# Optimization experiments

Hardware: AMD Instinct MI355X
Metric: run time of the kernel (lower is better)

The kernel has to match this reference:

```python
import jax, jax.numpy as jnp
import numpy as np

EPS_BN = 1e-5
EPS_LN = 1e-5

def _bn(x, g, b, m, v):
    # inference-mode BatchNorm2d over channel dim 1
    scale = g / jnp.sqrt(v + EPS_BN)
    return x * scale[None, :, None, None] + (b - m * scale)[None, :, None, None]

def _conv1x1(x, w, b=None):
    y = jnp.einsum('bchw,oc->bohw', x, w)
    if b is not None:
        y = y + b[None, :, None, None]
    return y

def _gelu(x):
    return jax.nn.gelu(x, approximate=False)

def setup_inputs() -> dict:
    key = jax.random.key(0)
    ks = jax.random.split(key, 40)
    B, C, H, W = 32, 160, 56, 56
    C5, C3 = C // 5, C * 3
    s = 0.05
    d = {}
    d['x'] = jax.random.normal(ks[0], (B, C, H, W), jnp.float32)
    d['bn1_g'] = jax.random.uniform(ks[1], (C,), jnp.float32, 0.5, 1.5)
    d['bn1_b'] = jax.random.normal(ks[2], (C,)) * s
    d['bn1_m'] = jax.random.normal(ks[3], (C,)) * s
    d['bn1_v'] = jnp.ones((C,), jnp.float32)
    names = ['t', 'b', 'r', 'l', 'c']
    for i, n in enumerate(names):
        d['w' + n] = jax.random.normal(ks[4 + i], (C5, C)) * s
        d['b' + n] = jax.random.normal(ks[9 + i], (C5,)) * s
    d['wf1'] = jax.random.normal(ks[14], (C, C)) * s
    d['bf1'] = jax.random.normal(ks[15], (C,)) * s
    d['bn2_g'] = jax.random.uniform(ks[16], (C,), jnp.float32, 0.5, 1.5)
    d['bn2_b'] = jax.random.normal(ks[17], (C,)) * s
    d['bn2_m'] = jax.random.normal(ks[18], (C,)) * s
    d['bn2_v'] = jnp.ones((C,), jnp.float32)
    d['wph'] = jax.random.normal(ks[19], (W, W)) * s
    d['bph'] = jax.random.normal(ks[20], (W,)) * s
    d['wpw'] = jax.random.normal(ks[21], (H, H)) * s
    d['bpw'] = jax.random.normal(ks[22], (H,)) * s
    d['wf2'] = jax.random.normal(ks[23], (C, C3)) * s
    d['ln_g'] = jax.random.uniform(ks[24], (C,), jnp.float32, 0.5, 1.5)
    d['ln_b'] = jax.random.normal(ks[25], (C,)) * s
    d['wfc1'] = jax.random.normal(ks[26], (C3, C)) * s
    d['bfc1'] = jax.random.normal(ks[27], (C3,)) * s
    d['wfc2'] = jax.random.normal(ks[28], (C, C3)) * s
    d['bfc2'] = jax.random.normal(ks[29], (C,)) * s
    d['step'] = 1
    return d

def reference(x, bn1_g, bn1_b, bn1_m, bn1_v, wt, bt, wb, bb, wr, br, wl, bl, wc, bc,
              wf1, bf1, bn2_g, bn2_b, bn2_m, bn2_v, wph, bph, wpw, bpw, wf2,
              ln_g, ln_b, wfc1, bfc1, wfc2, bfc2, step):
    B, C, H, W = x.shape
    # ---- localMix: ShiftedPillarsConcatentation_BNAct_NP5 ----
    h = _gelu(_bn(x, bn1_g, bn1_b, bn1_m, bn1_v))
    x_t = _conv1x1(h, wt, bt)
    x_b = _conv1x1(h, wb, bb)
    x_r = _conv1x1(h, wr, br)
    x_l = _conv1x1(h, wl, bl)
    x_c = _conv1x1(h, wc, bc)
    # pad then narrow exactly as torch: t/l shift by 1, b/r shift by step
    x_t = jnp.pad(x_t, ((0, 0), (0, 0), (0, step), (0, 0)))[:, :, 1:1 + H, :]
    x_b = jnp.pad(x_b, ((0, 0), (0, 0), (step, 0), (0, 0)))[:, :, 0:H, :]
    x_l = jnp.pad(x_l, ((0, 0), (0, 0), (0, 0), (0, step)))[:, :, :, 1:1 + W]
    x_r = jnp.pad(x_r, ((0, 0), (0, 0), (0, 0), (step, 0)))[:, :, :, 0:W]
    lm = _conv1x1(jnp.concatenate([x_t, x_b, x_r, x_l, x_c], axis=1), wf1, bf1)
    # ---- globalMix: sparseMLP_BNAct ----
    g = _gelu(_bn(lm, bn2_g, bn2_b, bn2_m, bn2_v))
    # proj_h mixes the W axis (input permuted to (B,W,C,H)), bias per output W
    x_h = jnp.einsum('bchw,vw->bchv', g, wph) + bph[None, None, None, :]
    # proj_w mixes the H axis (input permuted to (B,H,C,W)), bias per output H
    x_w = jnp.einsum('bchw,uh->bcuw', g, wpw) + bpw[None, None, :, None]
    gm = _conv1x1(jnp.concatenate([g, x_h, x_w], axis=1), wf2)  # no bias
    x1 = gm + x  # residual 1
    # ---- channelMix: LN + Mlp over channels ----
    y = jnp.transpose(x1, (0, 2, 3, 1))  # BHWC
    mu = jnp.mean(y, axis=-1, keepdims=True)
    var = jnp.mean(jnp.square(y - mu), axis=-1, keepdims=True)
    y = (y - mu) / jnp.sqrt(var + EPS_LN) * ln_g + ln_b
    y = _gelu(jnp.einsum('bhwc,fc->bhwf', y, wfc1) + bfc1)
    y = jnp.einsum('bhwf,cf->bhwc', y, wfc2) + bfc2
    return jnp.transpose(y, (0, 3, 1, 2)) + x1  # residual 2
```

## Files before the change

kernel.cpp:

```cpp
#include <hip/hip_runtime.h>
#include <hip/hip_bf16.h>
#include <math.h>

typedef __hip_bfloat16 bf16;
typedef __attribute__((ext_vector_type(8))) short s8v;
typedef __attribute__((ext_vector_type(4))) float f4v;
typedef __attribute__((ext_vector_type(4))) unsigned short u4v;

#define Bn  32
#define Cn  160
#define HWn 3136
#define Pn  100352

__device__ __forceinline__ float b2f(bf16 v){ return __bfloat162float(v); }
__device__ __forceinline__ bf16  f2b(float v){ return __float2bfloat16(v); }
__device__ __forceinline__ float bits2f(unsigned short u){
    union { float f; unsigned int i; } x; x.i = ((unsigned int)u) << 16; return x.f;
}
__device__ __forceinline__ unsigned short f2bits(float v){
    union { unsigned short us; bf16 b; } cv; cv.b = f2b(v); return cv.us;
}
__device__ __forceinline__ float gelu_f(float x){
    float ax = fabsf(x) * 0.7071067811865476f;
    float t  = 1.0f / (1.0f + 0.3275911f*ax);
    float p  = ((((1.061405429f*t - 1.453152027f)*t + 1.421413741f)*t
                 - 0.284496736f)*t + 0.254829592f)*t;
    float e  = __expf(-ax*ax);
    float erfv = 1.0f - p*e;
    float s = (x >= 0.f) ? erfv : -erfv;
    return 0.5f*x*(1.0f + s);
}

#define MFMA(a,b,c) __builtin_amdgcn_mfma_f32_16x16x32_bf16((a),(b),(c),0,0,0)

__global__ __launch_bounds__(256) void k0_prep(
    const float* __restrict__ wt, const float* __restrict__ wb_, const float* __restrict__ wr,
    const float* __restrict__ wl, const float* __restrict__ wc,
    const float* __restrict__ bt, const float* __restrict__ bb_, const float* __restrict__ br,
    const float* __restrict__ bl, const float* __restrict__ bc,
    const float* __restrict__ wf1, const float* __restrict__ bf1,
    const float* __restrict__ g2, const float* __restrict__ b2, const float* __restrict__ m2, const float* __restrict__ v2,
    const float* __restrict__ wf2, const float* __restrict__ wfc1, const float* __restrict__ wfc2,
    const float* __restrict__ wph, const float* __restrict__ wpw,
    const float* __restrict__ lng, const float* __restrict__ lnb, const float* __restrict__ bfc1,
    bf16* wcat, bf16* wf1b, bf16* wf2b, bf16* wfc1g, bf16* wfc2b, bf16* wphb, bf16* wpwb,
    float* bcat, float* epsv, float* eptv, float* wgs, float* wcb)
{
    int idx = blockIdx.x*256 + threadIdx.x;
    if (idx < 25600){ int o = idx/160, k = idx - o*160; int gi = o>>5, oo = o&31;
        const float* wp = gi==0?wt: gi==1?wb_: gi==2?wr: gi==3?wl: wc;
        wcat[idx] = f2b(wp[oo*160+k]); return; }
    idx -= 25600;
    if (idx < 25600){ wf1b[idx] = f2b(wf1[idx]); return; }
    idx -= 25600;
    if (idx < 76800){ wf2b[idx] = f2b(wf2[idx]); return; }
    idx -= 76800;
    if (idx < 76800){ int f = idx/160, c = idx - f*160;
        wfc1g[idx] = f2b(wfc1[f*160+c] * lng[c]); return; }
    idx -= 76800;
    if (idx < 76800){ wfc2b[idx] = f2b(wfc2[idx]); return; }
    idx -= 76800;
    if (idx < 4096){ int v = idx>>6, w = idx&63;
        wphb[idx] = (v<56 && w<56) ? f2b(wph[v*56+w]) : f2b(0.f); return; }
    idx -= 4096;
    if (idx < 4096){ int v = idx>>6, w = idx&63;
        wpwb[idx] = (v<56 && w<56) ? f2b(wpw[v*56+w]) : f2b(0.f); return; }
    idx -= 4096;
    if (idx < 160){ int o = idx; int gi = o>>5, oo = o&31;
        const float* bp = gi==0?bt: gi==1?bb_: gi==2?br: gi==3?bl: bc;
        bcat[o] = bp[oo]; return; }
    idx -= 160;
    if (idx < 160){ int o = idx; float s = g2[o]*rsqrtf(v2[o]+1e-5f);
        epsv[o] = s; eptv[o] = (bf1[o]-m2[o])*s + b2[o]; return; }
    idx -= 160;
    if (idx < 480){ int o = idx; float sg = 0.f, sb = 0.f;
        const float* wr_ = wfc1 + (size_t)o*160;
        for (int c = 0; c < 160; ++c){ float w = wr_[c]; sg += w*lng[c]; sb += w*lnb[c]; }
        wgs[o] = sg; wcb[o] = sb + bfc1[o]; return; }
}

__global__ __launch_bounds__(256) void k1_bn_gelu_tr(const float* __restrict__ x,
    const float* __restrict__ g, const float* __restrict__ b,
    const float* __restrict__ m, const float* __restrict__ v,
    bf16* __restrict__ hT)
{
    __shared__ float tile[64*161];
    __shared__ float sc[160], sh[160];
    int blk = blockIdx.x; int bb = blk/49; int hw0 = (blk - bb*49)*64;
    int tid = threadIdx.x;
    if (tid < 160){
        float s = g[tid] * rsqrtf(v[tid] + 1e-5f);
        sc[tid] = s; sh[tid] = b[tid] - m[tid]*s;
    }
    __syncthreads();
    const float* xb = x + (size_t)bb*Cn*HWn + hw0;
    for (int idx = tid; idx < 160*64; idx += 256){
        int c = idx >> 6, p = idx & 63;
        float val = xb[(size_t)c*HWn + p];
        tile[p*161 + c] = gelu_f(val*sc[c] + sh[c]);
    }
    __syncthreads();
    bf16* ho = hT + ((size_t)bb*HWn + hw0)*Cn;
    for (int idx = tid; idx < 64*160; idx += 256){
        int p = idx/160, c = idx - p*160;
        ho[idx] = f2b(tile[p*161 + c]);
    }
}

__global__ __launch_bounds__(256) void k2_conv5(const bf16* __restrict__ hT,
    const bf16* __restrict__ wcat, const float* __restrict__ bcat, bf16* __restrict__ y5T)
{
    __shared__ __align__(16) unsigned short Bs[2][16*168];
    int tid = threadIdx.x, wave = tid>>6, lane = tid&63, m = lane&15, q = lane>>4;
    size_t pos0 = (size_t)blockIdx.x*64;
    const unsigned short* Ap = (const unsigned short*)hT + (pos0 + wave*16 + m)*160 + q*8;
    s8v a[5];
    #pragma unroll
    for (int kb = 0; kb < 5; ++kb) a[kb] = *(const s8v*)(Ap + kb*32);
    { const s8v* sp = (const s8v*)((const unsigned short*)wcat);
      for (int c = tid; c < 320; c += 256){ int row = c/20, col = (c - row*20)*8;
          *(s8v*)&Bs[0][row*168 + col] = sp[c]; } }
    __syncthreads();
    for (int s = 0; s < 10; ++s){
        if (s+1 < 10){
            const s8v* sp = (const s8v*)((const unsigned short*)wcat + (size_t)(s+1)*2560);
            for (int c = tid; c < 320; c += 256){ int row = c/20, col = (c - row*20)*8;
                *(s8v*)&Bs[(s+1)&1][row*168 + col] = sp[c]; }
        }
        f4v acc = {0.f,0.f,0.f,0.f};
        const unsigned short* Bp = &Bs[s&1][m*168 + q*8];
        #pragma unroll
        for (int kb = 0; kb < 5; ++kb) acc = MFMA(a[kb], *(const s8v*)(Bp + kb*32), acc);
        float bias = bcat[s*16 + m];
        bf16* yo = y5T + (pos0 + wave*16 + q*4)*160 + s*16 + m;
        #pragma unroll
        for (int r = 0; r < 4; ++r) yo[r*160] = f2b(acc[r] + bias);
        __syncthreads();
    }
}

__global__ __launch_bounds__(256) void k3_wf1(const bf16* __restrict__ y5T,
    const bf16* __restrict__ wf1b, const float* __restrict__ epsv, const float* __restrict__ eptv,
    bf16* __restrict__ gT)
{
    __shared__ __align__(16) unsigned short Bs[2][16*168];
    int tid = threadIdx.x, wave = tid>>6, lane = tid&63, m = lane&15, q = lane>>4;
    int blk = blockIdx.x; int bb = blk/49; int hw0 = (blk - bb*49)*64;
    size_t pos0 = (size_t)bb*HWn + hw0;
    int phw = hw0 + wave*16 + m; int h = phw/56, w = phw - h*56;
    s8v a[5];
    #pragma unroll
    for (int kb = 0; kb < 5; ++kb){
        int h2 = h, w2 = w; bool ok = true;
        if      (kb == 0){ h2 = h+1; ok = (h2 < 56); }
        else if (kb == 1){ h2 = h-1; ok = (h2 >= 0); }
        else if (kb == 2){ w2 = w-1; ok = (w2 >= 0); }
        else if (kb == 3){ w2 = w+1; ok = (w2 < 56); }
        if (ok){
            const unsigned short* Ap = (const unsigned short*)y5T +
                ((size_t)bb*HWn + h2*56 + w2)*160 + kb*32 + q*8;
            a[kb] = *(const s8v*)Ap;
        } else {
            a[kb] = (s8v){0,0,0,0,0,0,0,0};
        }
    }
    { const s8v* sp = (const s8v*)((const unsigned short*)wf1b);
      for (int c = tid; c < 320; c += 256){ int row = c/20, col = (c - row*20)*8;
          *(s8v*)&Bs[0][row*168 + col] = sp[c]; } }
    __syncthreads();
    for (int s = 0; s < 10; ++s){
        if (s+1 < 10){
            const s8v* sp = (const s8v*)((const unsigned short*)wf1b + (size_t)(s+1)*2560);
            for (int c = tid; c < 320; c += 256){ int row = c/20, col = (c - row*20)*8;
                *(s8v*)&Bs[(s+1)&1][row*168 + col] = sp[c]; }
        }
        f4v acc = {0.f,0.f,0.f,0.f};
        const unsigned short* Bp = &Bs[s&1][m*168 + q*8];
        #pragma unroll
        for (int kb = 0; kb < 5; ++kb) acc = MFMA(a[kb], *(const s8v*)(Bp + kb*32), acc);
        int o = s*16 + m;
        float es = epsv[o], et = eptv[o];
        bf16* go = gT + (pos0 + wave*16 + q*4)*160 + o;
        #pragma unroll
        for (int r = 0; r < 4; ++r) go[r*160] = f2b(gelu_f(acc[r]*es + et));
        __syncthreads();
    }
}

__global__ __launch_bounds__(256) void k4_projh(const bf16* __restrict__ gT,
    const bf16* __restrict__ wphb, const float* __restrict__ bph, bf16* __restrict__ xhT)
{
    __shared__ __align__(16) unsigned short gS[160*72];
    int tid = threadIdx.x, wave = tid>>6, lane = tid&63, m = lane&15, q = lane>>4;
    int blk = blockIdx.x; int b = blk/56, h = blk - b*56;
    const unsigned short* ga = (const unsigned short*)gT + ((size_t)b*HWn + h*56)*160;
    for (int idx = tid; idx < 56*160; idx += 256){
        int w = idx/160, c = idx - w*160;
        gS[c*72 + w] = ga[idx];
    }
    for (int idx = tid; idx < 160*8; idx += 256){
        int c = idx>>3, w = 56 + (idx&7);
        gS[c*72 + w] = 0;
    }
    __syncthreads();
    int v0 = wave*16;
    s8v a[2];
    #pragma unroll
    for (int kb = 0; kb < 2; ++kb)
        a[kb] = *(const s8v*)((const unsigned short*)wphb + (v0+m)*64 + kb*32 + q*8);
    int v = v0 + q*4;
    for (int s = 0; s < 10; ++s){
        f4v acc = {0.f,0.f,0.f,0.f};
        const unsigned short* Bp = &gS[(s*16+m)*72 + q*8];
        #pragma unroll
        for (int kb = 0; kb < 2; ++kb) acc = MFMA(a[kb], *(const s8v*)(Bp + kb*32), acc);
        #pragma unroll
        for (int r = 0; r < 4; ++r){
            int vv = v + r;
            if (vv < 56)
                xhT[((size_t)b*HWn + h*56 + vv)*160 + s*16 + m] = f2b(acc[r] + bph[vv]);
        }
    }
}

__global__ __launch_bounds__(256) void k5_projw(const bf16* __restrict__ gT,
    const bf16* __restrict__ wpwb, const float* __restrict__ bpw, bf16* __restrict__ xwT)
{
    __shared__ __align__(16) unsigned short gS[160*72];
    int tid = threadIdx.x, wave = tid>>6, lane = tid&63, m = lane&15, q = lane>>4;
    int blk = blockIdx.x; int b = blk/56, w = blk - b*56;
    const unsigned short* gbase = (const unsigned short*)gT + ((size_t)b*HWn + w)*160;
    for (int idx = tid; idx < 56*160; idx += 256){
        int hh = idx/160, c = idx - hh*160;
        gS[c*72 + hh] = gbase[(size_t)hh*56*160 + c];
    }
    for (int idx = tid; idx < 160*8; idx += 256){
        int c = idx>>3, hh = 56 + (idx&7);
        gS[c*72 + hh] = 0;
    }
    __syncthreads();
    int v0 = wave*16;
    s8v a[2];
    #pragma unroll
    for (int kb = 0; kb < 2; ++kb)
        a[kb] = *(const s8v*)((const unsigned short*)wpwb + (v0+m)*64 + kb*32 + q*8);
    int v = v0 + q*4;
    for (int s = 0; s < 10; ++s){
        f4v acc = {0.f,0.f,0.f,0.f};
        const unsigned short* Bp = &gS[(s*16+m)*72 + q*8];
        #pragma unroll
        for (int kb = 0; kb < 2; ++kb) acc = MFMA(a[kb], *(const s8v*)(Bp + kb*32), acc);
        #pragma unroll
        for (int r = 0; r < 4; ++r){
            int vv = v + r;
            if (vv < 56)
                xwT[((size_t)b*HWn + vv*56 + w)*160 + s*16 + m] = f2b(acc[r] + bpw[vv]);
        }
    }
}

__global__ __launch_bounds__(256) void k6_wf2(const bf16* __restrict__ gT,
    const bf16* __restrict__ xhT, const bf16* __restrict__ xwT,
    const bf16* __restrict__ wf2b, bf16* __restrict__ gm)
{
    __shared__ __align__(16) unsigned short Bs[2][16*488];
    int tid = threadIdx.x, wave = tid>>6, lane = tid&63, m = lane&15, q = lane>>4;
    size_t pos0 = (size_t)blockIdx.x*64;
    size_t prow = (pos0 + wave*16 + m)*160;
    s8v a[15];
    #pragma unroll
    for (int kb = 0; kb < 15; ++kb){
        const bf16* src = (kb < 5) ? gT : (kb < 10 ? xhT : xwT);
        int kc = (kb - (kb < 5 ? 0 : (kb < 10 ? 5 : 10)))*32 + q*8;
        a[kb] = *(const s8v*)((const unsigned short*)src + prow + kc);
    }
    { const s8v* sp = (const s8v*)((const unsigned short*)wf2b);
      for (int c = tid; c < 960; c += 256){ int row = c/60, col = (c - row*60)*8;
          *(s8v*)&Bs[0][row*488 + col] = sp[c]; } }
    __syncthreads();
    for (int s = 0; s < 10; ++s){
        if (s+1 < 10){
            const s8v* sp = (const s8v*)((const unsigned short*)wf2b + (size_t)(s+1)*7680);
            for (int c = tid; c < 960; c += 256){ int row = c/60, col = (c - row*60)*8;
                *(s8v*)&Bs[(s+1)&1][row*488 + col] = sp[c]; }
        }
        f4v acc = {0.f,0.f,0.f,0.f};
        const unsigned short* Bp = &Bs[s&1][m*488 + q*8];
        #pragma unroll
        for (int kb = 0; kb < 15; ++kb) acc = MFMA(a[kb], *(const s8v*)(Bp + kb*32), acc);
        bf16* go = gm + (pos0 + wave*16 + q*4)*160 + s*16 + m;
        #pragma unroll
        for (int r = 0; r < 4; ++r) go[r*160] = f2b(acc[r]);
        __syncthreads();
    }
}

__global__ __launch_bounds__(256,3) void k78_mlp(const float* __restrict__ x,
    const bf16* __restrict__ gm,
    const bf16* __restrict__ wfc1g, const float* __restrict__ wcb,
    const bf16* __restrict__ wfc2b, const float* __restrict__ bfc2,
    float* __restrict__ out)
{
    __shared__ __align__(16) char lds[40960];
    float* Xs = (float*)lds;
    char* UsB = lds;
    char* AsB = lds + 30720;

    int tid = threadIdx.x, wave = tid>>6, lane = tid&63, m = lane&15, q = lane>>4;
    int rt = wave&1, chh = wave>>1;
    int blk = blockIdx.x; int bb = blk/98; int hw0 = (blk - bb*98)*32;
    size_t pos0 = (size_t)bb*HWn + hw0;
    const float* xb = x + (size_t)bb*Cn*HWn + hw0;

    for (int idx = tid; idx < 160*32; idx += 256){
        int c = idx >> 5, p = idx & 31;
        Xs[p*164 + c] = xb[(size_t)c*HWn + p];
    }
    __syncthreads();

    {
        int p = tid >> 3, q8 = tid & 7; int c0 = q8*20;
        const unsigned short* gp = (const unsigned short*)gm + (pos0 + p)*160 + c0;
        float y[20]; float s = 0.f, ss = 0.f;
        #pragma unroll
        for (int j = 0; j < 5; ++j){
            u4v gv = *(const u4v*)(gp + j*4);
            f4v xv = *(const f4v*)&Xs[p*164 + c0 + j*4];
            #pragma unroll
            for (int t = 0; t < 4; ++t){
                float vv = xv[t] + bits2f(gv[t]);
                y[j*4 + t] = vv; s += vv; ss += vv*vv;
            }
        }
        s += __shfl_xor(s, 1); ss += __shfl_xor(ss, 1);
        s += __shfl_xor(s, 2); ss += __shfl_xor(ss, 2);
        s += __shfl_xor(s, 4); ss += __shfl_xor(ss, 4);
        float mean = s * (1.f/160.f);
        float var  = ss * (1.f/160.f) - mean*mean;
        float rstd = rsqrtf(var + 1e-5f);
        int xr = (p&7)<<4;
        #pragma unroll
        for (int j = 0; j < 5; ++j){
            u4v pk;
            #pragma unroll
            for (int t = 0; t < 4; ++t) pk[t] = f2bits((y[j*4 + t] - mean)*rstd);
            int off = (p*320 + (c0 + j*4)*2) ^ xr;
            *(u4v*)(AsB + off) = pk;
        }
    }
    __syncthreads();

    {
        s8v a1[5];
        {
            int row = rt*16 + m; int xr = (row&7)<<4;
            #pragma unroll
            for (int kb = 0; kb < 5; ++kb){
                int off = (row*320 + (q*8 + kb*32)*2) ^ xr;
                a1[kb] = *(const s8v*)(AsB + off);
            }
        }
        const unsigned short* W1 = (const unsigned short*)wfc1g + ((size_t)chh*15*16 + m)*160 + q*8;
        s8v b0[5], b1[5];
        #pragma unroll
        for (int kb = 0; kb < 5; ++kb) b0[kb] = *(const s8v*)(W1 + kb*32);
        #pragma unroll
        for (int s = 0; s < 15; ++s){
            if (s + 1 < 15){
                const unsigned short* Wn = W1 + (size_t)(s+1)*2560;
                #pragma unroll
                for (int kb = 0; kb < 5; ++kb) b1[kb] = *(const s8v*)(Wn + kb*32);
            }
            f4v acc = {0.f,0.f,0.f,0.f};
            #pragma unroll
            for (int kb = 0; kb < 5; ++kb) acc = MFMA(a1[kb], b0[kb], acc);
            int o = (chh*15 + s)*16 + m;
            float wc = wcb[o];
            #pragma unroll
            for (int r = 0; r < 4; ++r){
                int row = rt*16 + q*4 + r;
                int off = (row*960 + o*2) ^ ((row&7)<<4);
                *(unsigned short*)(UsB + off) = f2bits(gelu_f(acc[r] + wc));
            }
            if (s + 1 < 15){
                #pragma unroll
                for (int kb = 0; kb < 5; ++kb) b0[kb] = b1[kb];
            }
        }
    }
    __syncthreads();

    {
        s8v a2[15];
        {
            int row = rt*16 + m; int xr = (row&7)<<4;
            #pragma unroll
            for (int kb = 0; kb < 15; ++kb){
                int off = (row*960 + (q*8 + kb*32)*2) ^ xr;
                a2[kb] = *(const s8v*)(UsB + off);
            }
        }
        #pragma unroll
        for (int s = 0; s < 5; ++s){
            int o = chh*80 + s*16 + m;
            const unsigned short* W2 = (const unsigned short*)wfc2b + (size_t)o*480 + q*8;
            s8v b2[15];
            #pragma unroll
            for (int kb = 0; kb < 15; ++kb) b2[kb] = *(const s8v*)(W2 + kb*32);
            f4v acc = {0.f,0.f,0.f,0.f};
            #pragma unroll
            for (int kb = 0; kb < 15; ++kb) acc = MFMA(a2[kb], b2[kb], acc);
            float bias = bfc2[o];
            const float* xp = x + (size_t)bb*Cn*HWn + (size_t)o*HWn + hw0 + rt*16 + q*4;
            f4v x4 = *(const f4v*)xp;
            const unsigned short* gmp = (const unsigned short*)gm + (pos0 + rt*16 + q*4)*160 + o;
            f4v o4;
            #pragma unroll
            for (int r = 0; r < 4; ++r)
                o4[r] = x4[r] + bits2f(gmp[(size_t)r*160]) + acc[r] + bias;
            float* op = out + (size_t)bb*Cn*HWn + (size_t)o*HWn + hw0 + rt*16 + q*4;
            *(f4v*)op = o4;
        }
    }
}

extern "C" void kernel_launch(void* const* d_in, const int* in_sizes, int n_in,
                              void* d_out, int out_size, void* d_ws, size_t ws_size,
                              hipStream_t stream)
{
    (void)in_sizes; (void)n_in; (void)out_size; (void)ws_size;
    const float* x     = (const float*)d_in[0];
    const float* bn1g  = (const float*)d_in[1];
    const float* bn1b  = (const float*)d_in[2];
    const float* bn1m  = (const float*)d_in[3];
    const float* bn1v  = (const float*)d_in[4];
    const float* wt    = (const float*)d_in[5];
    const float* bt    = (const float*)d_in[6];
    const float* wb    = (const float*)d_in[7];
    const float* bb    = (const float*)d_in[8];
    const float* wr    = (const float*)d_in[9];
    const float* br    = (const float*)d_in[10];
    const float* wl    = (const float*)d_in[11];
    const float* bl    = (const float*)d_in[12];
    const float* wc    = (const float*)d_in[13];
    const float* bc    = (const float*)d_in[14];
    const float* wf1   = (const float*)d_in[15];
    const float* bf1   = (const float*)d_in[16];
    const float* bn2g  = (const float*)d_in[17];
    const float* bn2b  = (const float*)d_in[18];
    const float* bn2m  = (const float*)d_in[19];
    const float* bn2v  = (const float*)d_in[20];
    const float* wph   = (const float*)d_in[21];
    const float* bph   = (const float*)d_in[22];
    const float* wpw   = (const float*)d_in[23];
    const float* bpw   = (const float*)d_in[24];
    const float* wf2   = (const float*)d_in[25];
    const float* lng   = (const float*)d_in[26];
    const float* lnb   = (const float*)d_in[27];
    const float* wfc1  = (const float*)d_in[28];
    const float* bfc1  = (const float*)d_in[29];
    const float* wfc2  = (const float*)d_in[30];
    const float* bfc2v = (const float*)d_in[31];
    float* outp = (float*)d_out;

    const size_t PC2 = (size_t)Pn*160*2;
    char* ws = (char*)d_ws;
    bf16* hT   = (bf16*)(ws + 0*PC2);
    bf16* y5T  = (bf16*)(ws + 1*PC2);
    bf16* gT   = (bf16*)(ws + 2*PC2);
    bf16* xhT  = (bf16*)(ws + 3*PC2);
    bf16* xwT  = (bf16*)(ws + 4*PC2);
    bf16* gm   = (bf16*)(ws + 5*PC2);
    char* wsw  = ws + 6*PC2;
    bf16*  wcat  = (bf16*)(wsw + 0);
    bf16*  wf1b  = (bf16*)(wsw + 51200);
    bf16*  wf2b  = (bf16*)(wsw + 102400);
    bf16*  wfc1g = (bf16*)(wsw + 256000);
    bf16*  wfc2b = (bf16*)(wsw + 409600);
    bf16*  wphb  = (bf16*)(wsw + 563200);
    bf16*  wpwb  = (bf16*)(wsw + 571392);
    float* bcat  = (float*)(wsw + 579584);
    float* epsv  = (float*)(wsw + 580224);
    float* eptv  = (float*)(wsw + 580864);
    float* wgs   = (float*)(wsw + 581504);
    float* wcb   = (float*)(wsw + 583424);

    const int GP = Pn/64;
    const int GS = Bn*56;
    const int GF = Pn/32;

    k0_prep<<<1136, 256, 0, stream>>>(wt, wb, wr, wl, wc, bt, bb, br, bl, bc,
                                      wf1, bf1, bn2g, bn2b, bn2m, bn2v,
                                      wf2, wfc1, wfc2, wph, wpw,
                                      lng, lnb, bfc1,
                                      wcat, wf1b, wf2b, wfc1g, wfc2b, wphb, wpwb,
                                      bcat, epsv, eptv, wgs, wcb);
    k1_bn_gelu_tr<<<GP, 256, 0, stream>>>(x, bn1g, bn1b, bn1m, bn1v, hT);
    k2_conv5     <<<GP, 256, 0, stream>>>(hT, wcat, bcat, y5T);
    k3_wf1       <<<GP, 256, 0, stream>>>(y5T, wf1b, epsv, eptv, gT);
    k4_projh     <<<GS, 256, 0, stream>>>(gT, wphb, bph, xhT);
    k5_projw     <<<GS, 256, 0, stream>>>(gT, wpwb, bpw, xwT);
    k6_wf2       <<<GP, 256, 0, stream>>>(gT, xhT, xwT, wf2b, gm);
    k78_mlp      <<<GF, 256, 0, stream>>>(x, gm, wfc1g, wcb, wfc2b, bfc2v, outp);
}
```

Measured before the change: 509.8 us.

## Fuse BN+GELU transpose into conv5 kernel and stage gm residual in LDS

Merges the BN1+GELU transpose kernel into the conv5 MFMA kernel. The activated tile is written as bf16 into swizzled LDS and MFMA A-fragments are loaded straight from there. This removes the hT round trip through global memory and one kernel launch. In the MLP kernel, the gm row already loaded for LayerNorm is also cached in extra LDS, replacing strided global reloads of gm in the epilogue. The cost is more LDS per block in both kernels, which may lower occupancy.

```diff
diff --git a/kernel.cpp b/kernel.cpp
--- a/kernel.cpp
+++ b/kernel.cpp
@@ -79,48 +79,43 @@
         wgs[o] = sg; wcb[o] = sb + bfc1[o]; return; }
 }
 
-__global__ __launch_bounds__(256) void k1_bn_gelu_tr(const float* __restrict__ x,
+__global__ __launch_bounds__(256) void k12_bn_conv5(const float* __restrict__ x,
     const float* __restrict__ g, const float* __restrict__ b,
-    const float* __restrict__ m, const float* __restrict__ v,
-    bf16* __restrict__ hT)
-{
-    __shared__ float tile[64*161];
+    const float* __restrict__ m_, const float* __restrict__ v,
+    const bf16* __restrict__ wcat, const float* __restrict__ bcat, bf16* __restrict__ y5T)
+{
+    __shared__ __align__(16) unsigned short Bs[2][16*168];
+    __shared__ __align__(16) char AsB[64*320];
     __shared__ float sc[160], sh[160];
+    int tid = threadIdx.x, wave = tid>>6, lane = tid&63, m = lane&15, q = lane>>4;
     int blk = blockIdx.x; int bb = blk/49; int hw0 = (blk - bb*49)*64;
-    int tid = threadIdx.x;
     if (tid < 160){
         float s = g[tid] * rsqrtf(v[tid] + 1e-5f);
-        sc[tid] = s; sh[tid] = b[tid] - m[tid]*s;
-    }
+        sc[tid] = s; sh[tid] = b[tid] - m_[tid]*s;
+    }
+    { const s8v* sp = (const s8v*)((const unsigned short*)wcat);
+      for (int c = tid; c < 320; c += 256){ int row = c/20, col = (c - row*20)*8;
+          *(s8v*)&Bs[0][row*168 + col] = sp[c]; } }
     __syncthreads();
     const float* xb = x + (size_t)bb*Cn*HWn + hw0;
     for (int idx = tid; idx < 160*64; idx += 256){
         int c = idx >> 6, p = idx & 63;
         float val = xb[(size_t)c*HWn + p];
-        tile[p*161 + c] = gelu_f(val*sc[c] + sh[c]);
-    }
-    __syncthreads();
-    bf16* ho = hT + ((size_t)bb*HWn + hw0)*Cn;
-    for (int idx = tid; idx < 64*160; idx += 256){
-        int p = idx/160, c = idx - p*160;
-        ho[idx] = f2b(tile[p*161 + c]);
-    }
-}
-
-__global__ __launch_bounds__(256) void k2_conv5(const bf16* __restrict__ hT,
-    const bf16* __restrict__ wcat, const float* __restrict__ bcat, bf16* __restrict__ y5T)
-{
-    __shared__ __align__(16) unsigned short Bs[2][16*168];
-    int tid = threadIdx.x, wave = tid>>6, lane = tid&63, m = lane&15, q = lane>>4;
-    size_t pos0 = (size_t)blockIdx.x*64;
-    const unsigned short* Ap = (const unsigned short*)hT + (pos0 + wave*16 + m)*160 + q*8;
+        unsigned short us = f2bits(gelu_f(val*sc[c] + sh[c]));
+        int off = (p*320 + c*2) ^ ((p&7)<<4);
+        *(unsigned short*)(AsB + off) = us;
+    }
+    __syncthreads();
+    size_t pos0 = (size_t)bb*HWn + hw0;
     s8v a[5];
-    #pragma unroll
-    for (int kb = 0; kb < 5; ++kb) a[kb] = *(const s8v*)(Ap + kb*32);
-    { const s8v* sp = (const s8v*)((const unsigned short*)wcat);
-      for (int c = tid; c < 320; c += 256){ int row = c/20, col = (c - row*20)*8;
-          *(s8v*)&Bs[0][row*168 + col] = sp[c]; } }
-    __syncthreads();
+    {
+        int row = wave*16 + m; int xr = (row&7)<<4;
+        #pragma unroll
+        for (int kb = 0; kb < 5; ++kb){
+            int off = (row*320 + (q*8 + kb*32)*2) ^ xr;
+            a[kb] = *(const s8v*)(AsB + off);
+        }
+    }
     for (int s = 0; s < 10; ++s){
         if (s+1 < 10){
             const s8v* sp = (const s8v*)((const unsigned short*)wcat + (size_t)(s+1)*2560);
@@ -301,10 +296,11 @@
     const bf16* __restrict__ wfc2b, const float* __restrict__ bfc2,
     float* __restrict__ out)
 {
-    __shared__ __align__(16) char lds[40960];
+    __shared__ __align__(16) char lds[51200];
     float* Xs = (float*)lds;
     char* UsB = lds;
     char* AsB = lds + 30720;
+    char* GsB = lds + 40960;
 
     int tid = threadIdx.x, wave = tid>>6, lane = tid&63, m = lane&15, q = lane>>4;
     int rt = wave&1, chh = wave>>1;
@@ -325,6 +321,7 @@
         #pragma unroll
         for (int j = 0; j < 5; ++j){
             u4v gv = *(const u4v*)(gp + j*4);
+            *(u4v*)(GsB + p*320 + (c0 + j*4)*2) = gv;
             f4v xv = *(const f4v*)&Xs[p*164 + c0 + j*4];
             #pragma unroll
             for (int t = 0; t < 4; ++t){
@@ -413,11 +410,13 @@
             float bias = bfc2[o];
             const float* xp = x + (size_t)bb*Cn*HWn + (size_t)o*HWn + hw0 + rt*16 + q*4;
             f4v x4 = *(const f4v*)xp;
-            const unsigned short* gmp = (const unsigned short*)gm + (pos0 + rt*16 + q*4)*160 + o;
             f4v o4;
             #pragma unroll
-            for (int r = 0; r < 4; ++r)
-                o4[r] = x4[r] + bits2f(gmp[(size_t)r*160]) + acc[r] + bias;
+            for (int r = 0; r < 4; ++r){
+                int row = rt*16 + q*4 + r;
+                float gmv = bits2f(*(const unsigned short*)(GsB + row*320 + o*2));
+                o4[r] = x4[r] + gmv + acc[r] + bias;
+            }
             float* op = out + (size_t)bb*Cn*HWn + (size_t)o*HWn + hw0 + rt*16 + q*4;
             *(f4v*)op = o4;
         }
@@ -465,7 +464,6 @@
 
     const size_t PC2 = (size_t)Pn*160*2;
     char* ws = (char*)d_ws;
-    bf16* hT   = (bf16*)(ws + 0*PC2);
     bf16* y5T  = (bf16*)(ws + 1*PC2);
     bf16* gT   = (bf16*)(ws + 2*PC2);
     bf16* xhT  = (bf16*)(ws + 3*PC2);
@@ -495,8 +493,7 @@
                                       lng, lnb, bfc1,
                                       wcat, wf1b, wf2b, wfc1g, wfc2b, wphb, wpwb,
                                       bcat, epsv, eptv, wgs, wcb);
-    k1_bn_gelu_tr<<<GP, 256, 0, stream>>>(x, bn1g, bn1b, bn1m, bn1v, hT);
-    k2_conv5     <<<GP, 256, 0, stream>>>(hT, wcat, bcat, y5T);
+    k12_bn_conv5 <<<GP, 256, 0, stream>>>(x, bn1g, bn1b, bn1m, bn1v, wcat, bcat, y5T);
     k3_wf1       <<<GP, 256, 0, stream>>>(y5T, wf1b, epsv, eptv, gT);
     k4_projh     <<<GS, 256, 0, stream>>>(gT, wphb, bph, xhT);
     k5_projw     <<<GS, 256, 0, stream>>>(gT, wpwb, bpw, xwT);
```

Result: faster. 482.9 us (-5.3%).
